# Kernel tuning notes

Hardware: AMD Instinct MI355X
Metric: run time of the kernel (lower is better)

Reference implementation:

```python
import jax, jax.numpy as jnp
import numpy as np
import math

EMB, HID, SEQ, BATCH, VOCAB, LAYERS = 512, 1024, 128, 64, 10000, 2


def setup_inputs() -> dict:
    key = jax.random.key(0)
    ks = jax.random.split(key, 8)
    bnd = math.sqrt(1.0 / HID)
    return {
        "inputs": jax.random.randint(ks[0], (SEQ, BATCH), 0, VOCAB),
        "hidden": jnp.zeros((LAYERS, BATCH, HID), jnp.float32),
        "emb": jax.random.uniform(ks[1], (VOCAB, EMB), jnp.float32, -0.1, 0.1),
        "W_x0": jax.random.uniform(ks[2], (EMB, HID), jnp.float32, -bnd, bnd),
        "W_x1": jax.random.uniform(ks[3], (HID, HID), jnp.float32, -bnd, bnd),
        "W_h": jax.random.uniform(ks[4], (LAYERS, HID, HID), jnp.float32, -bnd, bnd),
        "b_h": jax.random.uniform(ks[5], (LAYERS, HID), jnp.float32, -bnd, bnd),
        "W_out": jax.random.uniform(ks[6], (HID, VOCAB), jnp.float32, -0.1, 0.1),
        "b_out": jnp.zeros((VOCAB,), jnp.float32),
    }


def reference(inputs, hidden, emb, W_x0, W_x1, W_h, b_h, W_out, b_out):
    # Stacked vanilla RNN over time; dropout is identity (dp_keep_prob=1.0).
    scale = jnp.asarray(math.sqrt(EMB), jnp.float32)  # WordEmbedding * sqrt(n_units)

    def step(h, tok):
        # h: (L, B, H); tok: (B,)
        x = emb[tok] * scale                                   # (B, E)
        h0 = jnp.tanh(x @ W_x0 + h[0] @ W_h[0] + b_h[0])       # (B, H)
        h1 = jnp.tanh(h0 @ W_x1 + h[1] @ W_h[1] + b_h[1])      # (B, H)
        logits_t = h1 @ W_out + b_out                          # (B, V)
        return jnp.stack([h0, h1]), logits_t

    final_hidden, logits = jax.lax.scan(step, hidden, inputs)
    return logits, final_hidden
```

## Files before the change

### kernel.cpp

```cpp
#include <hip/hip_runtime.h>
#include <math.h>


typedef unsigned short u16;
typedef unsigned long long u64;
typedef __bf16 bf16x8 __attribute__((ext_vector_type(8)));
typedef float  f32x4  __attribute__((ext_vector_type(4)));
typedef unsigned int u32x4 __attribute__((ext_vector_type(4)));
typedef u16 u16x8 __attribute__((ext_vector_type(8)));

#define SEQ_ 128
#define B_   64
#define E_   512
#define H_   1024
#define V_   10000
#define VP_  10112
#define ROWS_ (SEQ_*B_)
#define BH_  (B_*H_)
#define LOGITS_ 81920000
#define FPS_ (129*32)

__device__ __forceinline__ u16 f2bf(float f) {
  unsigned u = __builtin_bit_cast(unsigned, f);
  u += 0x7fffu + ((u >> 16) & 1u);
  return (u16)(u >> 16);
}
__device__ __forceinline__ float bf2f(u16 h) {
  unsigned u = ((unsigned)h) << 16;
  return __builtin_bit_cast(float, u);
}
__device__ __forceinline__ void st64(void* p, u64 v) {
  __hip_atomic_store((u64*)p, v, __ATOMIC_RELAXED, __HIP_MEMORY_SCOPE_AGENT);
}
__device__ __forceinline__ u64 pk64(float a, float b) {
  return (u64)__builtin_bit_cast(unsigned, a) |
         ((u64)__builtin_bit_cast(unsigned, b) << 32);
}
__device__ __forceinline__ float tanh_fast(float x) {
  float e = __expf(2.0f * x);
  return 1.0f - 2.0f * __builtin_amdgcn_rcpf(e + 1.0f);
}
__device__ __forceinline__ unsigned ld_sc0(const unsigned* p) {
  unsigned v;
  asm volatile("global_load_dword %0, %1, off sc0\n\t"
               "s_waitcnt vmcnt(0)"
               : "=v"(v) : "v"(p) : "memory");
  return v;
}


__global__ __launch_bounds__(256)
void transpose_split(const float* __restrict__ in, u16* __restrict__ outHi,
                     u16* __restrict__ outLo, int K, int N, int NP)
{
  __shared__ float tile[32][33];
  const int n0 = blockIdx.x * 32, k0 = blockIdx.y * 32;
  const int x = threadIdx.x & 31;
  const int y = threadIdx.x >> 5;
  (void)NP;
#pragma unroll
  for (int i = 0; i < 4; ++i) {
    const int r = y * 4 + i;
    const int n = n0 + x;
    tile[r][x] = (n < N) ? in[(size_t)(k0 + r) * N + n] : 0.f;
  }
  __syncthreads();
#pragma unroll
  for (int i = 0; i < 4; ++i) {
    const int r = y * 4 + i;
    const int n = n0 + r;
    const int k = k0 + x;
    const float v = tile[x][r];
    const u16 hb = f2bf(v);
    outHi[(size_t)n * K + k] = hb;
    if (outLo) outLo[(size_t)n * K + k] = f2bf(v - bf2f(hb));
  }
}

__global__ __launch_bounds__(256)
void gather_x(const int* __restrict__ toks, const float* __restrict__ emb,
              u16* __restrict__ XBhi, u16* __restrict__ XBlo)
{
  const int tid = blockIdx.x * 256 + threadIdx.x;
  const int row = tid >> 6;
  const int c8 = (tid & 63) * 8;
  const int tok = toks[row];
  const float* e = emb + (size_t)tok * E_ + c8;
  u16x8 hv, lv;
#pragma unroll
  for (int j = 0; j < 8; ++j) {
    float f = e[j] * 22.627416997969522f;
    u16 hb = f2bf(f);
    hv[j] = hb;
    lv[j] = f2bf(f - bf2f(hb));
  }
  *(u16x8*)(XBhi + (size_t)row * E_ + c8) = hv;
  *(u16x8*)(XBlo + (size_t)row * E_ + c8) = lv;
}

__global__ __launch_bounds__(256)
void hid_cast(const float* __restrict__ h, u16* H0hi, u16* H0lo, u16* H1hi, u16* H1lo)
{
  const int tid = blockIdx.x * 256 + threadIdx.x;
  float v0 = h[tid], v1 = h[BH_ + tid];
  u16 a = f2bf(v0); H0hi[tid] = a; H0lo[tid] = f2bf(v0 - bf2f(a));
  u16 b = f2bf(v1); H1hi[tid] = b; H1lo[tid] = f2bf(v1 - bf2f(b));
}

template<int NPASS>
__global__ __launch_bounds__(256)
void gemm_bf16(const u16* __restrict__ Ahi, const u16* __restrict__ Alo,
               const u16* __restrict__ Bhi, const u16* __restrict__ Blo,
               const float* __restrict__ bias, float* __restrict__ C,
               int K, int Nreal, int ldc, int nbx, int nby)
{
  constexpr int LDT = 40;
  __shared__ u16 lds[(NPASS == 3 ? 4 : 2) * 128 * LDT];
  u16* As  = lds;
  u16* Bs  = lds + 128 * LDT;
  u16* As2 = (NPASS == 3) ? (lds + 2 * 128 * LDT) : lds;
  u16* Bs2 = (NPASS == 3) ? (lds + 3 * 128 * LDT) : lds;

  const int S = 8;
  int bid  = blockIdx.x;
  int scol = bid / (S * nby);
  int rem  = bid - scol * (S * nby);
  int w    = nbx - scol * S; if (w > S) w = S;
  int bx   = scol * S + rem % w;
  int by   = rem / w;
  const int m0 = by * 128, n0 = bx * 128;

  const int tid  = threadIdx.x;
  const int wave = tid >> 6, lane = tid & 63;
  const int wm = (wave & 1) * 64, wn = (wave >> 1) * 64;
  const int lrow = lane & 15, lk = (lane >> 4) * 8;

  f32x4 acc[4][4] = {};

  const int kTiles = K >> 5;
  for (int kt = 0; kt < kTiles; ++kt) {
    const int k0 = kt << 5;
    __syncthreads();
#pragma unroll
    for (int c = tid; c < 512; c += 256) {
      const int row = c >> 2, kq = c & 3;
      const int l = row * LDT + kq * 8;
      *(u32x4*)(As + l) = *(const u32x4*)(Ahi + (size_t)(m0 + row) * K + k0 + kq * 8);
      *(u32x4*)(Bs + l) = *(const u32x4*)(Bhi + (size_t)(n0 + row) * K + k0 + kq * 8);
      if constexpr (NPASS == 3) {
        *(u32x4*)(As2 + l) = *(const u32x4*)(Alo + (size_t)(m0 + row) * K + k0 + kq * 8);
        *(u32x4*)(Bs2 + l) = *(const u32x4*)(Blo + (size_t)(n0 + row) * K + k0 + kq * 8);
      }
    }
    __syncthreads();
    bf16x8 a[4], b[4];
#pragma unroll
    for (int i = 0; i < 4; ++i) {
      a[i] = *(const bf16x8*)(As + (wm + i * 16 + lrow) * LDT + lk);
      b[i] = *(const bf16x8*)(Bs + (wn + i * 16 + lrow) * LDT + lk);
    }
    if constexpr (NPASS == 3) {
      bf16x8 a2[4], b2[4];
#pragma unroll
      for (int i = 0; i < 4; ++i) {
        a2[i] = *(const bf16x8*)(As2 + (wm + i * 16 + lrow) * LDT + lk);
        b2[i] = *(const bf16x8*)(Bs2 + (wn + i * 16 + lrow) * LDT + lk);
      }
#pragma unroll
      for (int mi = 0; mi < 4; ++mi)
#pragma unroll
        for (int ni = 0; ni < 4; ++ni) {
          acc[mi][ni] = __builtin_amdgcn_mfma_f32_16x16x32_bf16(a[mi],  b[ni],  acc[mi][ni], 0, 0, 0);
          acc[mi][ni] = __builtin_amdgcn_mfma_f32_16x16x32_bf16(a[mi],  b2[ni], acc[mi][ni], 0, 0, 0);
          acc[mi][ni] = __builtin_amdgcn_mfma_f32_16x16x32_bf16(a2[mi], b[ni],  acc[mi][ni], 0, 0, 0);
        }
    } else {
#pragma unroll
      for (int mi = 0; mi < 4; ++mi)
#pragma unroll
        for (int ni = 0; ni < 4; ++ni)
          acc[mi][ni] = __builtin_amdgcn_mfma_f32_16x16x32_bf16(a[mi], b[ni], acc[mi][ni], 0, 0, 0);
    }
  }
#pragma unroll
  for (int mi = 0; mi < 4; ++mi)
#pragma unroll
    for (int ni = 0; ni < 4; ++ni)
#pragma unroll
      for (int r = 0; r < 4; ++r) {
        const int row = m0 + wm + mi * 16 + (lane >> 4) * 4 + r;
        const int col = n0 + wn + ni * 16 + lrow;
        if (col < Nreal) {
          float v = acc[mi][ni][r];
          if (bias) v += bias[col];
          C[(size_t)row * ldc + col] = v;
        }
      }
}

__device__ __forceinline__ void publishWG(unsigned* f, int wgi)
{
  asm volatile("s_waitcnt vmcnt(0)" ::: "memory");
  __syncthreads();
  if (threadIdx.x == 0)
    __hip_atomic_store(f + wgi, 1u, __ATOMIC_RELAXED, __HIP_MEMORY_SCOPE_AGENT);
}
__device__ __forceinline__ void pollL(const unsigned* f)
{
  if (threadIdx.x < 64) {
    const int l = threadIdx.x & 31;
    for (int it = 0;; ++it) {
      unsigned v;
      if ((it & 15) == 15)
        v = __hip_atomic_load(f + l, __ATOMIC_RELAXED, __HIP_MEMORY_SCOPE_AGENT);
      else
        v = ld_sc0(f + l);
      if (__all(v != 0)) break;
      __builtin_amdgcn_s_sleep(1);
    }
  }
  __syncthreads();
}
__device__ __forceinline__ void pollR(const unsigned* f)
{
  if (threadIdx.x < 64) {
    const int l = threadIdx.x & 31;
    int it = 0;
    for (;;) {
      unsigned v = __hip_atomic_load(f + l, __ATOMIC_RELAXED,
                                     __HIP_MEMORY_SCOPE_AGENT);
      if (__all(v != 0)) break;
      if (it < 4) __builtin_amdgcn_s_sleep(1);
      else        __builtin_amdgcn_s_sleep(4);
      ++it;
    }
  }
  __syncthreads();
}

__device__ __forceinline__ f32x4 gemm96(const u16* __restrict__ Ahi,
                                        const u16* __restrict__ Alo,
                                        const u16* bsp, int xorv, int lk8,
                                        size_t aoff, f32x4 acc0)
{
  f32x4 acc1 = {0.f, 0.f, 0.f, 0.f};
  f32x4 acc2 = {0.f, 0.f, 0.f, 0.f};
#pragma unroll
  for (int kc = 0; kc < 32; ++kc) {
    bf16x8 ah = *(const bf16x8*)(Ahi + aoff + kc * 32);
    bf16x8 al = *(const bf16x8*)(Alo + aoff + kc * 32);
    bf16x8 bh = *(const bf16x8*)(bsp + ((kc * 32 + lk8) ^ xorv));
    bf16x8 bl = *(const bf16x8*)(bsp + 32768 + ((kc * 32 + lk8) ^ xorv));
    acc0 = __builtin_amdgcn_mfma_f32_16x16x32_bf16(bh, ah, acc0, 0, 0, 0);
    acc1 = __builtin_amdgcn_mfma_f32_16x16x32_bf16(bl, ah, acc1, 0, 0, 0);
    acc2 = __builtin_amdgcn_mfma_f32_16x16x32_bf16(bh, al, acc2, 0, 0, 0);
  }
  return acc0 + acc1 + acc2;
}

__global__ __launch_bounds__(256, 1)
void recur_roles(const u16* __restrict__ Wh0h, const u16* __restrict__ Wh0l,
                 const u16* __restrict__ Wx1h, const u16* __restrict__ Wx1l,
                 const u16* __restrict__ Wh1h, const u16* __restrict__ Wh1l,
                 const float* __restrict__ XP0, const float* __restrict__ b1,
                 float* __restrict__ Pbuf,
                 u16* __restrict__ H0hi, u16* __restrict__ H0lo,
                 u16* __restrict__ H1hi, u16* __restrict__ H1lo,
                 float* __restrict__ final0, float* __restrict__ final1,
                 unsigned* __restrict__ flags)
{
  __shared__ u16 bsm[2 * 32 * 1024];

  const int bid  = blockIdx.x;
  const int xcd  = bid & 7;
  if (xcd >= 6) return;
  const int role = xcd >> 1;
  const int bg   = xcd & 1;
  const int cg   = bid >> 3;

  const u16* Bhi = (role == 0) ? Wh0h : (role == 1) ? Wx1h : Wh1h;
  const u16* Blo = (role == 0) ? Wh0l : (role == 1) ? Wx1l : Wh1l;

  const int tid  = threadIdx.x;
  const int wv   = tid >> 6, lane = tid & 63;
  const int wbg  = wv >> 1, wcg = wv & 1;
  const int lb   = lane & 15;
  const int lk8  = (lane >> 4) * 8;

  for (int c = tid; c < 8192; c += 256) {
    const int p   = c >> 12;
    const int cc  = c & 4095;
    const int col = cc >> 7;
    const int k8  = (cc & 127) * 8;
    u32x4 v = *(const u32x4*)((p ? Blo : Bhi) + (size_t)(cg * 32 + col) * H_ + k8);
    *(u32x4*)(bsm + p * 32768 + col * 1024 + (k8 ^ ((col & 7) << 3))) = v;
  }
  __syncthreads();

  const int batch = bg * 32 + wbg * 16 + lb;
  const int c0    = cg * 32 + wcg * 16 + (lk8 >> 1);
  const int colL  = wcg * 16 + lb;
  const int xorv  = (colL & 7) << 3;
  const u16* bsp  = bsm + colL * 1024;
  const size_t aoff = (size_t)batch * H_ + lk8;
  const size_t boff = (size_t)batch * H_ + c0;

  unsigned* flg0 = flags;
  unsigned* flgP = flags + 2 * FPS_;
  unsigned* flg1 = flags + 4 * FPS_;

  if (role == 0) {
    for (int t = 0; t < SEQ_; ++t) {
      f32x4 init = *(const f32x4*)(XP0 + (size_t)t * BH_ + boff);
      if (t >= 1) pollL(flg0 + ((size_t)bg * 129 + t) * 32);
      f32x4 acc = gemm96(H0hi + (size_t)t * BH_, H0lo + (size_t)t * BH_,
                         bsp, xorv, lk8, aoff, init);
      u64 whi = 0, wlo = 0; float hv[4];
#pragma unroll
      for (int r = 0; r < 4; ++r) {
        float v = tanh_fast(acc[r]);
        u16 hb = f2bf(v);
        whi |= (u64)hb << (16 * r);
        wlo |= (u64)f2bf(v - bf2f(hb)) << (16 * r);
        hv[r] = v;
      }
      st64(H0hi + (size_t)(t + 1) * BH_ + boff, whi);
      st64(H0lo + (size_t)(t + 1) * BH_ + boff, wlo);
      if (t == SEQ_ - 1) {
        st64(final0 + boff,     pk64(hv[0], hv[1]));
        st64(final0 + boff + 2, pk64(hv[2], hv[3]));
      }
      publishWG(flg0 + ((size_t)bg * 129 + (t + 1)) * 32, cg);
    }
  } else if (role == 1) {
    const f32x4 binit = *(const f32x4*)(b1 + c0);
    for (int s = 1; s <= SEQ_; ++s) {
      pollR(flg0 + ((size_t)bg * 129 + s) * 32);
      f32x4 acc = gemm96(H0hi + (size_t)s * BH_, H0lo + (size_t)s * BH_,
                         bsp, xorv, lk8, aoff, binit);
      float* op = Pbuf + (size_t)(s - 1) * BH_ + boff;
      st64(op,     pk64(acc[0], acc[1]));
      st64(op + 2, pk64(acc[2], acc[3]));
      publishWG(flgP + ((size_t)bg * 129 + s) * 32, cg);
    }
  } else {
    for (int s = 1; s <= SEQ_; ++s) {
      pollR(flgP + ((size_t)bg * 129 + s) * 32);
      if (s >= 2) pollL(flg1 + ((size_t)bg * 129 + (s - 1)) * 32);
      f32x4 init = *(const f32x4*)(Pbuf + (size_t)(s - 1) * BH_ + boff);
      f32x4 acc = gemm96(H1hi + (size_t)(s - 1) * BH_, H1lo + (size_t)(s - 1) * BH_,
                         bsp, xorv, lk8, aoff, init);
      u64 whi = 0, wlo = 0; float hv[4];
#pragma unroll
      for (int r = 0; r < 4; ++r) {
        float v = tanh_fast(acc[r]);
        u16 hb = f2bf(v);
        whi |= (u64)hb << (16 * r);
        wlo |= (u64)f2bf(v - bf2f(hb)) << (16 * r);
        hv[r] = v;
      }
      st64(H1hi + (size_t)s * BH_ + boff, whi);
      st64(H1lo + (size_t)s * BH_ + boff, wlo);
      if (s == SEQ_) {
        st64(final1 + boff,     pk64(hv[0], hv[1]));
        st64(final1 + boff + 2, pk64(hv[2], hv[3]));
      }
      publishWG(flg1 + ((size_t)bg * 129 + s) * 32, cg);
    }
  }
}

extern "C" void kernel_launch(void* const* d_in, const int* in_sizes, int n_in,
                              void* d_out, int out_size, void* d_ws, size_t ws_size,
                              hipStream_t stream)
{
  (void)in_sizes; (void)n_in; (void)out_size; (void)ws_size;
  const int*   toks = (const int*)d_in[0];
  const float* hid0 = (const float*)d_in[1];
  const float* emb  = (const float*)d_in[2];
  const float* Wx0  = (const float*)d_in[3];
  const float* Wx1  = (const float*)d_in[4];
  const float* Wh   = (const float*)d_in[5];
  const float* bh   = (const float*)d_in[6];
  const float* Wout = (const float*)d_in[7];
  const float* bout = (const float*)d_in[8];
  float* out = (float*)d_out;

  char* ws = (char*)d_ws;
  size_t off = 0;
  auto alloc = [&](size_t bytes) -> void* {
    void* p = ws + off;
    off += (bytes + 255) & ~(size_t)255;
    return p;
  };
  unsigned* flags = (unsigned*)alloc(6 * FPS_ * 4);
  u16* XBhi  = (u16*)alloc((size_t)ROWS_ * E_ * 2);
  u16* XBlo  = (u16*)alloc((size_t)ROWS_ * E_ * 2);
  u16* Wx0Th = (u16*)alloc((size_t)H_ * E_ * 2);
  u16* Wx0Tl = (u16*)alloc((size_t)H_ * E_ * 2);
  u16* Wx1Th = (u16*)alloc((size_t)H_ * H_ * 2);
  u16* Wx1Tl = (u16*)alloc((size_t)H_ * H_ * 2);
  u16* Wh0Th = (u16*)alloc((size_t)H_ * H_ * 2);
  u16* Wh0Tl = (u16*)alloc((size_t)H_ * H_ * 2);
  u16* Wh1Th = (u16*)alloc((size_t)H_ * H_ * 2);
  u16* Wh1Tl = (u16*)alloc((size_t)H_ * H_ * 2);
  u16* WoutT = (u16*)alloc((size_t)VP_ * H_ * 2);
  float* XP0 = (float*)alloc((size_t)ROWS_ * H_ * 4);
  float* Pbuf= (float*)alloc((size_t)SEQ_ * BH_ * 4);
  u16* H0hi  = (u16*)alloc((size_t)(SEQ_ + 1) * BH_ * 2);
  u16* H0lo  = (u16*)alloc((size_t)(SEQ_ + 1) * BH_ * 2);
  u16* H1hi  = (u16*)alloc((size_t)(SEQ_ + 1) * BH_ * 2);
  u16* H1lo  = (u16*)alloc((size_t)(SEQ_ + 1) * BH_ * 2);

  hipMemsetAsync(flags, 0, 6 * FPS_ * 4, stream);
  transpose_split<<<dim3(H_ / 32, E_ / 32), 256, 0, stream>>>(Wx0, Wx0Th, Wx0Tl, E_, H_, H_);
  transpose_split<<<dim3(H_ / 32, H_ / 32), 256, 0, stream>>>(Wx1, Wx1Th, Wx1Tl, H_, H_, H_);
  transpose_split<<<dim3(H_ / 32, H_ / 32), 256, 0, stream>>>(Wh,           Wh0Th, Wh0Tl, H_, H_, H_);
  transpose_split<<<dim3(H_ / 32, H_ / 32), 256, 0, stream>>>(Wh + H_ * H_, Wh1Th, Wh1Tl, H_, H_, H_);
  transpose_split<<<dim3(VP_ / 32, H_ / 32), 256, 0, stream>>>(Wout, WoutT, nullptr, H_, V_, VP_);
  gather_x<<<ROWS_ * E_ / 8 / 256, 256, 0, stream>>>(toks, emb, XBhi, XBlo);
  hid_cast<<<BH_ / 256, 256, 0, stream>>>(hid0, H0hi, H0lo, H1hi, H1lo);

  gemm_bf16<3><<<8 * 64, 256, 0, stream>>>(XBhi, XBlo, Wx0Th, Wx0Tl, bh, XP0,
                                           E_, H_, H_, 8, 64);
  recur_roles<<<256, 256, 0, stream>>>(Wh0Th, Wh0Tl, Wx1Th, Wx1Tl, Wh1Th, Wh1Tl,
                                       XP0, bh + H_, Pbuf,
                                       H0hi, H0lo, H1hi, H1lo,
                                       out + LOGITS_, out + LOGITS_ + BH_, flags);
  gemm_bf16<1><<<79 * 64, 256, 0, stream>>>(H1hi + BH_, nullptr, WoutT, nullptr,
                                            bout, out, H_, V_, V_, 79, 64);
}
```

Before: 1.890 ms.

## Split recurrent roles into 16-column strips with intra-block split-K reduction

Doubles the recurrent kernel grid so each workgroup owns 16 output columns instead of 32. The four waves are split across two batch halves and two K halves, with partial sums reduced through shared memory. Activation loads are hoisted into registers ahead of the MFMA loop. Flag arrays widen to 64 entries per step and the polls check all 64 lanes, with backoff sleep added to pollL. The intent is to spread the serial per-step GEMM over more CUs and shorten per-step latency, at the cost of more flags to poll and an extra block barrier each step.

Result: slower. 2.230 ms (+18.0%).

```diff
diff --git a/kernel.cpp b/kernel.cpp
--- a/kernel.cpp
+++ b/kernel.cpp
@@ -18,7 +18,7 @@
 #define ROWS_ (SEQ_*B_)
 #define BH_  (B_*H_)
 #define LOGITS_ 81920000
-#define FPS_ (129*32)
+#define FPS_ (129*64)
 
 __device__ __forceinline__ u16 f2bf(float f) {
   unsigned u = __builtin_bit_cast(unsigned, f);
@@ -42,8 +42,7 @@
 }
 __device__ __forceinline__ unsigned ld_sc0(const unsigned* p) {
   unsigned v;
-  asm volatile("global_load_dword %0, %1, off sc0\n\t"
-               "s_waitcnt vmcnt(0)"
+  asm volatile("global_load_dword %0, %1, off sc0\n\ts_waitcnt vmcnt(0)"
                : "=v"(v) : "v"(p) : "memory");
   return v;
 }
@@ -208,7 +207,7 @@
 __device__ __forceinline__ void pollL(const unsigned* f)
 {
   if (threadIdx.x < 64) {
-    const int l = threadIdx.x & 31;
+    const int l = threadIdx.x;
     for (int it = 0;; ++it) {
       unsigned v;
       if ((it & 15) == 15)
@@ -216,7 +215,7 @@
       else
         v = ld_sc0(f + l);
       if (__all(v != 0)) break;
-      __builtin_amdgcn_s_sleep(1);
+      if (it < 4) __builtin_amdgcn_s_sleep(1); else __builtin_amdgcn_s_sleep(4);
     }
   }
   __syncthreads();
@@ -224,41 +223,45 @@
 __device__ __forceinline__ void pollR(const unsigned* f)
 {
   if (threadIdx.x < 64) {
-    const int l = threadIdx.x & 31;
+    const int l = threadIdx.x;
     int it = 0;
     for (;;) {
       unsigned v = __hip_atomic_load(f + l, __ATOMIC_RELAXED,
                                      __HIP_MEMORY_SCOPE_AGENT);
       if (__all(v != 0)) break;
-      if (it < 4) __builtin_amdgcn_s_sleep(1);
-      else        __builtin_amdgcn_s_sleep(4);
+      if (it < 4) __builtin_amdgcn_s_sleep(1); else __builtin_amdgcn_s_sleep(4);
       ++it;
     }
   }
   __syncthreads();
 }
 
-__device__ __forceinline__ f32x4 gemm96(const u16* __restrict__ Ahi,
+__device__ __forceinline__ f32x4 gemm48(const u16* __restrict__ Ahi,
                                         const u16* __restrict__ Alo,
                                         const u16* bsp, int xorv, int lk8,
-                                        size_t aoff, f32x4 acc0)
-{
+                                        int kbase, size_t aoff, f32x4 acc0)
+{
+  bf16x8 ah[16], al[16];
+#pragma unroll
+  for (int kc = 0; kc < 16; ++kc) {
+    ah[kc] = *(const bf16x8*)(Ahi + aoff + kc * 32);
+    al[kc] = *(const bf16x8*)(Alo + aoff + kc * 32);
+  }
   f32x4 acc1 = {0.f, 0.f, 0.f, 0.f};
   f32x4 acc2 = {0.f, 0.f, 0.f, 0.f};
 #pragma unroll
-  for (int kc = 0; kc < 32; ++kc) {
-    bf16x8 ah = *(const bf16x8*)(Ahi + aoff + kc * 32);
-    bf16x8 al = *(const bf16x8*)(Alo + aoff + kc * 32);
-    bf16x8 bh = *(const bf16x8*)(bsp + ((kc * 32 + lk8) ^ xorv));
-    bf16x8 bl = *(const bf16x8*)(bsp + 32768 + ((kc * 32 + lk8) ^ xorv));
-    acc0 = __builtin_amdgcn_mfma_f32_16x16x32_bf16(bh, ah, acc0, 0, 0, 0);
-    acc1 = __builtin_amdgcn_mfma_f32_16x16x32_bf16(bl, ah, acc1, 0, 0, 0);
-    acc2 = __builtin_amdgcn_mfma_f32_16x16x32_bf16(bh, al, acc2, 0, 0, 0);
+  for (int kc = 0; kc < 16; ++kc) {
+    const int kidx = (kbase + kc * 32 + lk8) ^ xorv;
+    bf16x8 bh = *(const bf16x8*)(bsp + kidx);
+    bf16x8 bl = *(const bf16x8*)(bsp + 16384 + kidx);
+    acc0 = __builtin_amdgcn_mfma_f32_16x16x32_bf16(bh, ah[kc], acc0, 0, 0, 0);
+    acc1 = __builtin_amdgcn_mfma_f32_16x16x32_bf16(bl, ah[kc], acc1, 0, 0, 0);
+    acc2 = __builtin_amdgcn_mfma_f32_16x16x32_bf16(bh, al[kc], acc2, 0, 0, 0);
   }
   return acc0 + acc1 + acc2;
 }
 
-__global__ __launch_bounds__(256, 1)
+__global__ __launch_bounds__(256, 2)
 void recur_roles(const u16* __restrict__ Wh0h, const u16* __restrict__ Wh0l,
                  const u16* __restrict__ Wx1h, const u16* __restrict__ Wx1l,
                  const u16* __restrict__ Wh1h, const u16* __restrict__ Wh1l,
@@ -269,41 +272,44 @@
                  float* __restrict__ final0, float* __restrict__ final1,
                  unsigned* __restrict__ flags)
 {
-  __shared__ u16 bsm[2 * 32 * 1024];
-
-  const int bid  = blockIdx.x;
-  const int xcd  = bid & 7;
+  __shared__ u16 bsm[2 * 16 * 1024];
+  __shared__ float psum[2][64][4];
+
+  const int bid   = blockIdx.x;
+  const int xcd   = bid & 7;
   if (xcd >= 6) return;
-  const int role = xcd >> 1;
-  const int bg   = xcd & 1;
-  const int cg   = bid >> 3;
+  const int role  = xcd >> 1;
+  const int bg    = xcd & 1;
+  const int strip = bid >> 3;
 
   const u16* Bhi = (role == 0) ? Wh0h : (role == 1) ? Wx1h : Wh1h;
   const u16* Blo = (role == 0) ? Wh0l : (role == 1) ? Wx1l : Wh1l;
 
   const int tid  = threadIdx.x;
   const int wv   = tid >> 6, lane = tid & 63;
-  const int wbg  = wv >> 1, wcg = wv & 1;
+  const int wbg  = wv & 1, kv = wv >> 1;
   const int lb   = lane & 15;
   const int lk8  = (lane >> 4) * 8;
 
-  for (int c = tid; c < 8192; c += 256) {
-    const int p   = c >> 12;
-    const int cc  = c & 4095;
+  for (int c = tid; c < 4096; c += 256) {
+    const int p   = c >> 11;
+    const int cc  = c & 2047;
     const int col = cc >> 7;
     const int k8  = (cc & 127) * 8;
-    u32x4 v = *(const u32x4*)((p ? Blo : Bhi) + (size_t)(cg * 32 + col) * H_ + k8);
-    *(u32x4*)(bsm + p * 32768 + col * 1024 + (k8 ^ ((col & 7) << 3))) = v;
+    u32x4 v = *(const u32x4*)((p ? Blo : Bhi) + (size_t)(strip * 16 + col) * H_ + k8);
+    *(u32x4*)(bsm + p * 16384 + col * 1024 + (k8 ^ ((col & 7) << 3))) = v;
   }
   __syncthreads();
 
   const int batch = bg * 32 + wbg * 16 + lb;
-  const int c0    = cg * 32 + wcg * 16 + (lk8 >> 1);
-  const int colL  = wcg * 16 + lb;
+  const int c0    = strip * 16 + (lk8 >> 1);
+  const int colL  = lb;
   const int xorv  = (colL & 7) << 3;
   const u16* bsp  = bsm + colL * 1024;
-  const size_t aoff = (size_t)batch * H_ + lk8;
+  const int kbase = kv * 512;
+  const size_t aoff = (size_t)batch * H_ + kbase + lk8;
   const size_t boff = (size_t)batch * H_ + c0;
+  const f32x4 zero4 = {0.f, 0.f, 0.f, 0.f};
 
   unsigned* flg0 = flags;
   unsigned* flgP = flags + 2 * FPS_;
@@ -311,61 +317,77 @@
 
   if (role == 0) {
     for (int t = 0; t < SEQ_; ++t) {
-      f32x4 init = *(const f32x4*)(XP0 + (size_t)t * BH_ + boff);
-      if (t >= 1) pollL(flg0 + ((size_t)bg * 129 + t) * 32);
-      f32x4 acc = gemm96(H0hi + (size_t)t * BH_, H0lo + (size_t)t * BH_,
-                         bsp, xorv, lk8, aoff, init);
-      u64 whi = 0, wlo = 0; float hv[4];
-#pragma unroll
-      for (int r = 0; r < 4; ++r) {
-        float v = tanh_fast(acc[r]);
-        u16 hb = f2bf(v);
-        whi |= (u64)hb << (16 * r);
-        wlo |= (u64)f2bf(v - bf2f(hb)) << (16 * r);
-        hv[r] = v;
-      }
-      st64(H0hi + (size_t)(t + 1) * BH_ + boff, whi);
-      st64(H0lo + (size_t)(t + 1) * BH_ + boff, wlo);
-      if (t == SEQ_ - 1) {
-        st64(final0 + boff,     pk64(hv[0], hv[1]));
-        st64(final0 + boff + 2, pk64(hv[2], hv[3]));
-      }
-      publishWG(flg0 + ((size_t)bg * 129 + (t + 1)) * 32, cg);
+      f32x4 init = (kv == 0) ? *(const f32x4*)(XP0 + (size_t)t * BH_ + boff) : zero4;
+      if (t >= 1) pollL(flg0 + ((size_t)bg * 129 + t) * 64);
+      f32x4 acc = gemm48(H0hi + (size_t)t * BH_, H0lo + (size_t)t * BH_,
+                         bsp, xorv, lk8, kbase, aoff, init);
+      if (kv == 1) *(f32x4*)&psum[wbg][lane][0] = acc;
+      __syncthreads();
+      if (kv == 0) {
+        acc += *(const f32x4*)&psum[wbg][lane][0];
+        u64 whi = 0, wlo = 0; float hv[4];
+#pragma unroll
+        for (int r = 0; r < 4; ++r) {
+          float v = tanh_fast(acc[r]);
+          u16 hb = f2bf(v);
+          whi |= (u64)hb << (16 * r);
+          wlo |= (u64)f2bf(v - bf2f(hb)) << (16 * r);
+          hv[r] = v;
+        }
+        st64(H0hi + (size_t)(t + 1) * BH_ + boff, whi);
+        st64(H0lo + (size_t)(t + 1) * BH_ + boff, wlo);
+        if (t == SEQ_ - 1) {
+          st64(final0 + boff,     pk64(hv[0], hv[1]));
+          st64(final0 + boff + 2, pk64(hv[2], hv[3]));
+        }
+      }
+      publishWG(flg0 + ((size_t)bg * 129 + (t + 1)) * 64, strip);
     }
   } else if (role == 1) {
-    const f32x4 binit = *(const f32x4*)(b1 + c0);
+    const f32x4 binit = (kv == 0) ? *(const f32x4*)(b1 + c0) : zero4;
     for (int s = 1; s <= SEQ_; ++s) {
-      pollR(flg0 + ((size_t)bg * 129 + s) * 32);
-      f32x4 acc = gemm96(H0hi + (size_t)s * BH_, H0lo + (size_t)s * BH_,
-                         bsp, xorv, lk8, aoff, binit);
-      float* op = Pbuf + (size_t)(s - 1) * BH_ + boff;
-      st64(op,     pk64(acc[0], acc[1]));
-      st64(op + 2, pk64(acc[2], acc[3]));
-      publishWG(flgP + ((size_t)bg * 129 + s) * 32, cg);
+      pollR(flg0 + ((size_t)bg * 129 + s) * 64);
+      f32x4 acc = gemm48(H0hi + (size_t)s * BH_, H0lo + (size_t)s * BH_,
+                         bsp, xorv, lk8, kbase, aoff, binit);
+      if (kv == 1) *(f32x4*)&psum[wbg][lane][0] = acc;
+      __syncthreads();
+      if (kv == 0) {
+        acc += *(const f32x4*)&psum[wbg][lane][0];
+        float* op = Pbuf + (size_t)(s - 1) * BH_ + boff;
+        st64(op,     pk64(acc[0], acc[1]));
+        st64(op + 2, pk64(acc[2], acc[3]));
+      }
+      publishWG(flgP + ((size_t)bg * 129 + s) * 64, strip);
     }
   } else {
     for (int s = 1; s <= SEQ_; ++s) {
-      pollR(flgP + ((size_t)bg * 129 + s) * 32);
-      if (s >= 2) pollL(flg1 + ((size_t)bg * 129 + (s - 1)) * 32);
-      f32x4 init = *(const f32x4*)(Pbuf + (size_t)(s - 1) * BH_ + boff);
-      f32x4 acc = gemm96(H1hi + (size_t)(s - 1) * BH_, H1lo + (size_t)(s - 1) * BH_,
-                         bsp, xorv, lk8, aoff, init);
-      u64 whi = 0, wlo = 0; float hv[4];
-#pragma unroll
-      for (int r = 0; r < 4; ++r) {
-        float v = tanh_fast(acc[r]);
-        u16 hb = f2bf(v);
-        whi |= (u64)hb << (16 * r);
-        wlo |= (u64)f2bf(v - bf2f(hb)) << (16 * r);
-        hv[r] = v;
-      }
-      st64(H1hi + (size_t)s * BH_ + boff, whi);
-      st64(H1lo + (size_t)s * BH_ + boff, wlo);
-      if (s == SEQ_) {
-        st64(final1 + boff,     pk64(hv[0], hv[1]));
-        st64(final1 + boff + 2, pk64(hv[2], hv[3]));
-      }
-      publishWG(flg1 + ((size_t)bg * 129 + s) * 32, cg);
+      pollR(flgP + ((size_t)bg * 129 + s) * 64);
+      if (s >= 2) pollL(flg1 + ((size_t)bg * 129 + (s - 1)) * 64);
+      f32x4 init = (kv == 0) ? *(const f32x4*)(Pbuf + (size_t)(s - 1) * BH_ + boff)
+                             : zero4;
+      f32x4 acc = gemm48(H1hi + (size_t)(s - 1) * BH_, H1lo + (size_t)(s - 1) * BH_,
+                         bsp, xorv, lk8, kbase, aoff, init);
+      if (kv == 1) *(f32x4*)&psum[wbg][lane][0] = acc;
+      __syncthreads();
+      if (kv == 0) {
+        acc += *(const f32x4*)&psum[wbg][lane][0];
+        u64 whi = 0, wlo = 0; float hv[4];
+#pragma unroll
+        for (int r = 0; r < 4; ++r) {
+          float v = tanh_fast(acc[r]);
+          u16 hb = f2bf(v);
+          whi |= (u64)hb << (16 * r);
+          wlo |= (u64)f2bf(v - bf2f(hb)) << (16 * r);
+          hv[r] = v;
+        }
+        st64(H1hi + (size_t)s * BH_ + boff, whi);
+        st64(H1lo + (size_t)s * BH_ + boff, wlo);
+        if (s == SEQ_) {
+          st64(final1 + boff,     pk64(hv[0], hv[1]));
+          st64(final1 + boff + 2, pk64(hv[2], hv[3]));
+        }
+      }
+      publishWG(flg1 + ((size_t)bg * 129 + s) * 64, strip);
     }
   }
 }
@@ -423,7 +445,7 @@
 
   gemm_bf16<3><<<8 * 64, 256, 0, stream>>>(XBhi, XBlo, Wx0Th, Wx0Tl, bh, XP0,
                                            E_, H_, H_, 8, 64);
-  recur_roles<<<256, 256, 0, stream>>>(Wh0Th, Wh0Tl, Wx1Th, Wx1Tl, Wh1Th, Wh1Tl,
+  recur_roles<<<512, 256, 0, stream>>>(Wh0Th, Wh0Tl, Wx1Th, Wx1Tl, Wh1Th, Wh1Tl,
                                        XP0, bh + H_, Pbuf,
                                        H0hi, H0lo, H1hi, H1lo,
                                        out + LOGITS_, out + LOGITS_ + BH_, flags);
```
